# Kernel optimization log

Measured on AMD Instinct MI355X. Metric: run time of the kernel, lower is better.

The kernel has to match this reference:

```python
import jax, jax.numpy as jnp
from jax import lax
import numpy as np

STEPSZ = 0.1
ALPHA = 0.01
BETA = 0.01
FLTRSTD = 2.0
NSTEPS = 20
DMAX = 15.0
EXTGRADFAC = 10.0
CHUNK = 32  # node chunk size for distance-map render


def _gauss_edge_fltr(std):
    # Gaussian-derivative edge filters, one per spatial axis: [2, 1, K, K]
    r = int(np.ceil(3 * std))
    x = np.arange(-r, r + 1, dtype=np.float32)
    g = np.exp(-x ** 2 / (2 * std ** 2)).astype(np.float32)
    g /= g.sum()
    dg = (-x / std ** 2) * g
    f0 = np.outer(dg, g)   # d/d(axis0)
    f1 = np.outer(g, dg)   # d/d(axis1)
    return np.stack([f0, f1])[:, None].astype(np.float32)


def _snake_matrix(n, alpha, beta, stepsz):
    # implicit internal-energy step matrix (I + t*(alpha*D2 + beta*D2@D2))^-1, open chain
    D = 2 * np.eye(n) - np.eye(n, k=1) - np.eye(n, k=-1)
    D[0, 0] = 1.0
    D[-1, -1] = 1.0
    A = alpha * D + beta * (D @ D)
    return np.linalg.inv(np.eye(n) + stepsz * A).astype(np.float32)


def _bilerp(img, pts):
    # img [H,W], pts [N,2] (row, col) -> [N]
    H, W = img.shape
    r = jnp.clip(pts[:, 0], 0.0, H - 1.0)
    c = jnp.clip(pts[:, 1], 0.0, W - 1.0)
    r0 = jnp.floor(r).astype(jnp.int32)
    c0 = jnp.floor(c).astype(jnp.int32)
    r1 = jnp.minimum(r0 + 1, H - 1)
    c1 = jnp.minimum(c0 + 1, W - 1)
    fr = r - r0
    fc = c - c0
    return (img[r0, c0] * (1 - fr) * (1 - fc) + img[r1, c0] * fr * (1 - fc)
            + img[r0, c1] * (1 - fr) * fc + img[r1, c1] * fr * fc)


def setup_inputs() -> dict:
    key = jax.random.key(0)
    k1, k2, k3 = jax.random.split(key, 3)
    B, H, W, N = 8, 512, 512, 256
    pred_dmap = jax.random.normal(k1, (B, 1, H, W), dtype=jnp.float32)
    node_pos = jax.random.uniform(k2, (B, N, 2), dtype=jnp.float32) * jnp.array([H - 1.0, W - 1.0], dtype=jnp.float32)
    widths = jax.random.uniform(k3, (B, N), dtype=jnp.float32) * 3.0 + 1.0
    return {"pred_dmap": pred_dmap, "node_pos": node_pos, "widths": widths}


def reference(pred_dmap, node_pos, widths):
    B, _, H, W = pred_dmap.shape
    N = node_pos.shape[1]

    # gradient image: conv with Gaussian-derivative filters, scaled (cmptGradIm)
    fltr = jnp.asarray(_gauss_edge_fltr(FLTRSTD))
    gimg = lax.conv_general_dilated(
        pred_dmap, fltr, (1, 1), 'SAME',
        dimension_numbers=('NCHW', 'OIHW', 'NCHW')) * EXTGRADFAC  # [B,2,H,W]

    M = jnp.asarray(_snake_matrix(N, ALPHA, BETA, STEPSZ))  # [N,N]

    def force(g, pts):  # g [2,H,W], pts [N,2] -> [N,2]
        return jnp.stack([_bilerp(g[0], pts), _bilerp(g[1], pts)], axis=-1)

    force_b = jax.vmap(force)
    bounds = jnp.array([H - 1.0, W - 1.0], dtype=pred_dmap.dtype)

    def opt_step(pos, _):
        f = force_b(gimg, pos)                                   # [B,N,2]
        pos = jnp.einsum('nm,bmd->bnd', M, pos + STEPSZ * f)
        pos = jnp.clip(pos, 0.0, bounds)
        return pos, None

    pos, _ = lax.scan(opt_step, node_pos, None, length=NSTEPS)

    ys = jnp.arange(H, dtype=pred_dmap.dtype)
    xs = jnp.arange(W, dtype=pred_dmap.dtype)

    def render(p, w):  # p [N,2], w [N] -> [H,W]
        pc = p.reshape(N // CHUNK, CHUNK, 2)
        wc = w.reshape(N // CHUNK, CHUNK)

        def rstep(carry, pw):
            pp, ww = pw  # [C,2], [C]
            d = jnp.sqrt((ys[None, :, None] - pp[:, 0, None, None]) ** 2
                         + (xs[None, None, :] - pp[:, 1, None, None]) ** 2) - ww[:, None, None]
            return jnp.minimum(carry, d.min(0)), None

        dm, _ = lax.scan(rstep, jnp.full((H, W), DMAX, dtype=p.dtype), (pc, wc))
        return jnp.clip(dm, 0.0, DMAX)

    snake_dm = jax.vmap(render)(pos, widths)[:, None]  # [B,1,H,W]
    snake_dm = lax.stop_gradient(snake_dm)             # torch.no_grad in original
    return jnp.mean((pred_dmap - snake_dm) ** 2)
```

## Files before the change

### kernel.cpp

```cpp
#include <hip/hip_runtime.h>
#include <hip/hip_bf16.h>
#include <math.h>

#define HH 512
#define WW 512
#define NB 8
#define NN 256
#define KR 6
#define KS 13

struct MBand { float c[NN][17]; };

constexpr double Dd_c(int i, int j) {
    if (i < 0 || i >= NN || j < 0 || j >= NN) return 0.0;
    if (i == j) return (i == 0 || i == NN - 1) ? 1.0 : 2.0;
    int d = i - j;
    if (d == 1 || d == -1) return -1.0;
    return 0.0;
}

constexpr MBand make_mband() {
    MBand mb{};
    double xb[NN][5] = {};
    for (int n = 0; n < NN; ++n)
        for (int d = 0; d < 5; ++d) {
            int j = n + d - 2;
            double d2 = 0.0;
            for (int k = n - 1; k <= n + 1; ++k) d2 += Dd_c(n, k) * Dd_c(k, j);
            xb[n][d] = 0.1 * (0.01 * Dd_c(n, j) + 0.01 * d2);
        }
    for (int n = 0; n < NN; ++n) {
        double acc[17] = {};
        double cur[17] = {};
        acc[8] = 1.0; cur[8] = 1.0;
        double sign = -1.0;
        for (int k = 1; k <= 4; ++k) {
            double nxt[17] = {};
            int lo = -2 * k, hi = 2 * k;
            for (int tp = lo; tp <= hi; ++tp) {
                int j = n + tp;
                double s = 0.0;
                if (j >= 0 && j < NN) {
                    for (int t = tp - 2; t <= tp + 2; ++t) {
                        if (t < -8 || t > 8) continue;
                        int m = n + t;
                        if (m < 0 || m >= NN) continue;
                        s += cur[8 + t] * xb[m][(tp - t) + 2];
                    }
                }
                nxt[8 + tp] = s;
            }
            for (int q = 0; q < 17; ++q) { cur[q] = nxt[q]; acc[q] += sign * nxt[q]; }
            sign = -sign;
        }
        for (int q = 0; q < 17; ++q) mb.c[n][q] = (float)acc[q];
    }
    return mb;
}

__device__ __constant__ MBand d_mband = make_mband();

union GPix { unsigned u; struct { __hip_bfloat16 x, y; } h; };

__global__ __launch_bounds__(256) void conv_kernel(const float* __restrict__ pred,
                                                   unsigned* __restrict__ gimg,
                                                   float* __restrict__ out) {
    __shared__ float tin[44][44];
    __shared__ float midG[44][32];
    __shared__ float midD[44][32];

    const int b    = blockIdx.x & 7;
    const int tile = blockIdx.x >> 3;
    const int ty0  = (tile >> 4) * 32;
    const int tx0  = (tile & 15) * 32;
    const int t    = threadIdx.x;

    if (blockIdx.x == 0 && t == 0) out[0] = 0.f;

    float g[KS], dg[KS];
    float s = 0.f;
#pragma unroll
    for (int i = 0; i < KS; ++i) {
        float x = (float)(i - KR);
        g[i] = expf(-x * x / 8.f);
        s += g[i];
    }
#pragma unroll
    for (int i = 0; i < KS; ++i) {
        g[i] /= s;
        dg[i] = (-(float)(i - KR) / 4.f) * g[i];
    }

    const float* img = pred + (size_t)b * HH * WW;

    for (int idx = t; idx < 44 * 44; idx += 256) {
        int ly = idx / 44, lx = idx % 44;
        int gy = ty0 + ly - KR, gx = tx0 + lx - KR;
        float v = 0.f;
        if (gy >= 0 && gy < HH && gx >= 0 && gx < WW) v = img[gy * WW + gx];
        tin[ly][lx] = v;
    }
    __syncthreads();

    for (int idx = t; idx < 44 * 32; idx += 256) {
        int ly = idx / 32, ox = idx % 32;
        float aG = 0.f, aD = 0.f;
#pragma unroll
        for (int k = 0; k < KS; ++k) {
            float v = tin[ly][ox + k];
            aG += v * g[k];
            aD += v * dg[k];
        }
        midG[ly][ox] = aG;
        midD[ly][ox] = aD;
    }
    __syncthreads();

    unsigned* outp = gimg + (size_t)b * HH * WW;
    for (int idx = t; idx < 32 * 32; idx += 256) {
        int oy = idx / 32, ox = idx % 32;
        float a0 = 0.f, a1 = 0.f;
#pragma unroll
        for (int k = 0; k < KS; ++k) {
            a0 += midG[oy + k][ox] * dg[k];
            a1 += midD[oy + k][ox] * g[k];
        }
        GPix p;
        p.h.x = __float2bfloat16(10.f * a0);
        p.h.y = __float2bfloat16(10.f * a1);
        outp[(ty0 + oy) * WW + (tx0 + ox)] = p.u;
    }
}

__global__ __launch_bounds__(64, 1) void snake_kernel(const unsigned* __restrict__ gimg,
                                                      const float* __restrict__ node_pos,
                                                      float* __restrict__ pos_out) {
    const int batch = blockIdx.x & 7;
    const int chunk = blockIdx.x >> 3;
    const int l = threadIdx.x;
    const int nidx = chunk * 32 - 8 + l;
    const int cidx = min(max(nidx, 0), NN - 1);

    const unsigned* gp = gimg + (size_t)batch * HH * WW;

    float2 pp = ((const float2*)node_pos)[batch * NN + cidx];
    float p0 = pp.x, p1 = pp.y;

    float mbc[17];
#pragma unroll
    for (int t = 0; t < 17; ++t) mbc[t] = d_mband.c[cidx][t];

    for (int step = 0; step < 20; ++step) {
        float r = fminf(fmaxf(p0, 0.f), (float)(HH - 1));
        float c = fminf(fmaxf(p1, 0.f), (float)(WW - 1));
        float rf = floorf(r), cf = floorf(c);
        int r0 = (int)rf, c0 = (int)cf;
        int r1 = min(r0 + 1, HH - 1), c1 = min(c0 + 1, WW - 1);
        float fr = r - rf, fc = c - cf;
        GPix v00, v01, v10, v11;
        v00.u = gp[r0 * WW + c0];
        v01.u = gp[r0 * WW + c1];
        v10.u = gp[r1 * WW + c0];
        v11.u = gp[r1 * WW + c1];
        float w00 = (1.f - fr) * (1.f - fc), w01 = (1.f - fr) * fc;
        float w10 = fr * (1.f - fc),         w11 = fr * fc;
        float f0 = w00 * __bfloat162float(v00.h.x) + w01 * __bfloat162float(v01.h.x)
                 + w10 * __bfloat162float(v10.h.x) + w11 * __bfloat162float(v11.h.x);
        float f1 = w00 * __bfloat162float(v00.h.y) + w01 * __bfloat162float(v01.h.y)
                 + w10 * __bfloat162float(v10.h.y) + w11 * __bfloat162float(v11.h.y);
        float q0 = p0 + 0.1f * f0;
        float q1 = p1 + 0.1f * f1;

        float a0 = mbc[8] * q0;
        float a1 = mbc[8] * q1;
#pragma unroll
        for (int d = 1; d <= 8; ++d) {
            float u0 = __shfl_up(q0, d),   u1 = __shfl_up(q1, d);
            float w0 = __shfl_down(q0, d), w1 = __shfl_down(q1, d);
            a0 += mbc[8 - d] * u0 + mbc[8 + d] * w0;
            a1 += mbc[8 - d] * u1 + mbc[8 + d] * w1;
        }
        p0 = fminf(fmaxf(a0, 0.f), (float)(HH - 1));
        p1 = fminf(fmaxf(a1, 0.f), (float)(WW - 1));
    }

    if (l >= 8 && l < 40)
        ((float2*)pos_out)[batch * NN + nidx] = make_float2(p0, p1);
}

__global__ __launch_bounds__(256) void render_loss_kernel(const float* __restrict__ pred,
                                                          const float* __restrict__ pos,
                                                          const float* __restrict__ widths,
                                                          float* __restrict__ out) {
    __shared__ float sl0[NN], sl1[NN], slw[NN];
    __shared__ int cnt;
    __shared__ float wred[4];

    const int b    = blockIdx.x & 7;
    const int tile = blockIdx.x >> 3;
    const int ty0  = (tile >> 4) * 32;
    const int tx0  = (tile & 15) * 32;
    const int t    = threadIdx.x;

    if (t == 0) cnt = 0;
    __syncthreads();

    {
        float p0 = pos[(b * NN + t) * 2 + 0];
        float p1 = pos[(b * NN + t) * 2 + 1];
        float w  = widths[b * NN + t];
        float dy = fmaxf(fmaxf((float)ty0 - p0, p0 - (float)(ty0 + 31)), 0.f);
        float dx = fmaxf(fmaxf((float)tx0 - p1, p1 - (float)(tx0 + 31)), 0.f);
        float rr = 15.f + w;
        if (dy * dy + dx * dx <= rr * rr) {
            int i = atomicAdd(&cnt, 1);
            sl0[i] = p0; sl1[i] = p1; slw[i] = w;
        }
    }
    __syncthreads();
    const int c = cnt;

    const int oy = t >> 3;
    const int ox = (t & 7) * 4;
    const float fy = (float)(ty0 + oy);
    const float fx = (float)(tx0 + ox);

    float dm0 = 15.f, dm1 = 15.f, dm2 = 15.f, dm3 = 15.f;
    for (int j = 0; j < c; ++j) {
        float dy  = fy - sl0[j];
        float dy2 = dy * dy;
        float w   = slw[j];
        float dx  = fx - sl1[j];
        dm0 = fminf(dm0, __builtin_amdgcn_sqrtf(dy2 + dx * dx) - w);
        dx += 1.f;
        dm1 = fminf(dm1, __builtin_amdgcn_sqrtf(dy2 + dx * dx) - w);
        dx += 1.f;
        dm2 = fminf(dm2, __builtin_amdgcn_sqrtf(dy2 + dx * dx) - w);
        dx += 1.f;
        dm3 = fminf(dm3, __builtin_amdgcn_sqrtf(dy2 + dx * dx) - w);
    }
    dm0 = fminf(fmaxf(dm0, 0.f), 15.f);
    dm1 = fminf(fmaxf(dm1, 0.f), 15.f);
    dm2 = fminf(fmaxf(dm2, 0.f), 15.f);
    dm3 = fminf(fmaxf(dm3, 0.f), 15.f);

    const float4 pv = *(const float4*)(pred + (size_t)b * HH * WW
                                       + (ty0 + oy) * WW + (tx0 + ox));
    float e0 = pv.x - dm0, e1 = pv.y - dm1, e2 = pv.z - dm2, e3 = pv.w - dm3;
    float acc = (e0 * e0 + e1 * e1 + e2 * e2 + e3 * e3)
              * (1.0f / (float)(NB * HH * WW));

#pragma unroll
    for (int m = 1; m < 64; m <<= 1) acc += __shfl_xor(acc, m);
    if ((t & 63) == 0) wred[t >> 6] = acc;
    __syncthreads();
    if (t == 0) atomicAdd(out, wred[0] + wred[1] + wred[2] + wred[3]);
}

extern "C" void kernel_launch(void* const* d_in, const int* in_sizes, int n_in,
                              void* d_out, int out_size, void* d_ws, size_t ws_size,
                              hipStream_t stream) {
    const float* pred     = (const float*)d_in[0];
    const float* node_pos = (const float*)d_in[1];
    const float* widths   = (const float*)d_in[2];
    float* out = (float*)d_out;

    unsigned* gimg = (unsigned*)d_ws;
    float* pos_out = (float*)d_ws + (size_t)NB * HH * WW;

    conv_kernel<<<NB * 256, 256, 0, stream>>>(pred, gimg, out);

    snake_kernel<<<NB * 8, 64, 0, stream>>>(gimg, node_pos, pos_out);

    render_loss_kernel<<<NB * 256, 256, 0, stream>>>(pred, pos_out, widths, out);
}
```

Baseline: 54.26 us.

## Fuse snake optimization into render kernel with ticket-ordered global-atomic handoff

Merges the snake iteration kernel and the render/loss kernel into one launch. The first 64 blocks, assigned in order through a global ticket counter, run the snake chunks and signal per-batch completion counters. All blocks then spin until their batch's eight chunks are done before rendering. The last block to finish resets the counters. This removes one kernel launch and the gap between launches, and lets render blocks for finished batches start early. In exchange it adds spin-waiting, depends on ticket ordering to avoid deadlock, and keeps global state that persists across calls.

```diff
diff --git a/kernel.cpp b/kernel.cpp
--- a/kernel.cpp
+++ b/kernel.cpp
@@ -8,6 +8,7 @@
 #define NN 256
 #define KR 6
 #define KS 13
+#define NBLK (NB * 256)
 
 struct MBand { float c[NN][17]; };
 
@@ -62,6 +63,10 @@
 
 union GPix { unsigned u; struct { __hip_bfloat16 x, y; } h; };
 
+__device__ unsigned g_ticket = 0;
+__device__ unsigned g_chunk_done[NB] = {};
+__device__ unsigned g_all_done = 0;
+
 __global__ __launch_bounds__(256) void conv_kernel(const float* __restrict__ pred,
                                                    unsigned* __restrict__ gimg,
                                                    float* __restrict__ out) {
@@ -132,129 +137,169 @@
     }
 }
 
-__global__ __launch_bounds__(64, 1) void snake_kernel(const unsigned* __restrict__ gimg,
-                                                      const float* __restrict__ node_pos,
-                                                      float* __restrict__ pos_out) {
-    const int batch = blockIdx.x & 7;
-    const int chunk = blockIdx.x >> 3;
-    const int l = threadIdx.x;
-    const int nidx = chunk * 32 - 8 + l;
-    const int cidx = min(max(nidx, 0), NN - 1);
-
-    const unsigned* gp = gimg + (size_t)batch * HH * WW;
-
-    float2 pp = ((const float2*)node_pos)[batch * NN + cidx];
-    float p0 = pp.x, p1 = pp.y;
-
-    float mbc[17];
-#pragma unroll
-    for (int t = 0; t < 17; ++t) mbc[t] = d_mband.c[cidx][t];
-
-    for (int step = 0; step < 20; ++step) {
-        float r = fminf(fmaxf(p0, 0.f), (float)(HH - 1));
-        float c = fminf(fmaxf(p1, 0.f), (float)(WW - 1));
-        float rf = floorf(r), cf = floorf(c);
-        int r0 = (int)rf, c0 = (int)cf;
-        int r1 = min(r0 + 1, HH - 1), c1 = min(c0 + 1, WW - 1);
-        float fr = r - rf, fc = c - cf;
-        GPix v00, v01, v10, v11;
-        v00.u = gp[r0 * WW + c0];
-        v01.u = gp[r0 * WW + c1];
-        v10.u = gp[r1 * WW + c0];
-        v11.u = gp[r1 * WW + c1];
-        float w00 = (1.f - fr) * (1.f - fc), w01 = (1.f - fr) * fc;
-        float w10 = fr * (1.f - fc),         w11 = fr * fc;
-        float f0 = w00 * __bfloat162float(v00.h.x) + w01 * __bfloat162float(v01.h.x)
-                 + w10 * __bfloat162float(v10.h.x) + w11 * __bfloat162float(v11.h.x);
-        float f1 = w00 * __bfloat162float(v00.h.y) + w01 * __bfloat162float(v01.h.y)
-                 + w10 * __bfloat162float(v10.h.y) + w11 * __bfloat162float(v11.h.y);
-        float q0 = p0 + 0.1f * f0;
-        float q1 = p1 + 0.1f * f1;
-
-        float a0 = mbc[8] * q0;
-        float a1 = mbc[8] * q1;
-#pragma unroll
-        for (int d = 1; d <= 8; ++d) {
-            float u0 = __shfl_up(q0, d),   u1 = __shfl_up(q1, d);
-            float w0 = __shfl_down(q0, d), w1 = __shfl_down(q1, d);
-            a0 += mbc[8 - d] * u0 + mbc[8 + d] * w0;
-            a1 += mbc[8 - d] * u1 + mbc[8 + d] * w1;
-        }
-        p0 = fminf(fmaxf(a0, 0.f), (float)(HH - 1));
-        p1 = fminf(fmaxf(a1, 0.f), (float)(WW - 1));
-    }
-
-    if (l >= 8 && l < 40)
-        ((float2*)pos_out)[batch * NN + nidx] = make_float2(p0, p1);
-}
-
-__global__ __launch_bounds__(256) void render_loss_kernel(const float* __restrict__ pred,
-                                                          const float* __restrict__ pos,
-                                                          const float* __restrict__ widths,
-                                                          float* __restrict__ out) {
+__global__ __launch_bounds__(256) void snake_render_kernel(const float* __restrict__ pred,
+                                                           const unsigned* __restrict__ gimg,
+                                                           const float* __restrict__ node_pos,
+                                                           const float* __restrict__ widths,
+                                                           float* __restrict__ pos_out,
+                                                           float* __restrict__ out) {
     __shared__ float sl0[NN], sl1[NN], slw[NN];
     __shared__ int cnt;
     __shared__ float wred[4];
+    __shared__ unsigned s_ticket;
 
     const int b    = blockIdx.x & 7;
     const int tile = blockIdx.x >> 3;
-    const int ty0  = (tile >> 4) * 32;
-    const int tx0  = (tile & 15) * 32;
     const int t    = threadIdx.x;
 
-    if (t == 0) cnt = 0;
+    if (t == 0)
+        s_ticket = __hip_atomic_fetch_add(&g_ticket, 1u, __ATOMIC_RELAXED,
+                                          __HIP_MEMORY_SCOPE_AGENT);
     __syncthreads();
+    const unsigned tk = s_ticket;
+
+    if (tk < 64u) {
+        const int batch_s = tk & 7;
+        const int chunk   = tk >> 3;
+        if (t < 64) {
+            const int l = t;
+            const int nidx = chunk * 32 - 8 + l;
+            const int cidx = min(max(nidx, 0), NN - 1);
+
+            const unsigned* gp = gimg + (size_t)batch_s * HH * WW;
+
+            float2 pp = ((const float2*)node_pos)[batch_s * NN + cidx];
+            float p0 = pp.x, p1 = pp.y;
+
+            float mbc[17];
+#pragma unroll
+            for (int k = 0; k < 17; ++k) mbc[k] = d_mband.c[cidx][k];
+
+            for (int step = 0; step < 20; ++step) {
+                float r = fminf(fmaxf(p0, 0.f), (float)(HH - 1));
+                float c = fminf(fmaxf(p1, 0.f), (float)(WW - 1));
+                float rf = floorf(r), cf = floorf(c);
+                int r0 = (int)rf, c0 = (int)cf;
+                int r1 = min(r0 + 1, HH - 1), c1 = min(c0 + 1, WW - 1);
+                float fr = r - rf, fc = c - cf;
+                GPix v00, v01, v10, v11;
+                v00.u = gp[r0 * WW + c0];
+                v01.u = gp[r0 * WW + c1];
+                v10.u = gp[r1 * WW + c0];
+                v11.u = gp[r1 * WW + c1];
+                float w00 = (1.f - fr) * (1.f - fc), w01 = (1.f - fr) * fc;
+                float w10 = fr * (1.f - fc),         w11 = fr * fc;
+                float f0 = w00 * __bfloat162float(v00.h.x) + w01 * __bfloat162float(v01.h.x)
+                         + w10 * __bfloat162float(v10.h.x) + w11 * __bfloat162float(v11.h.x);
+                float f1 = w00 * __bfloat162float(v00.h.y) + w01 * __bfloat162float(v01.h.y)
+                         + w10 * __bfloat162float(v10.h.y) + w11 * __bfloat162float(v11.h.y);
+                float q0 = p0 + 0.1f * f0;
+                float q1 = p1 + 0.1f * f1;
+
+                float a0 = mbc[8] * q0;
+                float a1 = mbc[8] * q1;
+#pragma unroll
+                for (int d = 1; d <= 8; ++d) {
+                    float u0 = __shfl_up(q0, d),   u1 = __shfl_up(q1, d);
+                    float w0 = __shfl_down(q0, d), w1 = __shfl_down(q1, d);
+                    a0 += mbc[8 - d] * u0 + mbc[8 + d] * w0;
+                    a1 += mbc[8 - d] * u1 + mbc[8 + d] * w1;
+                }
+                p0 = fminf(fmaxf(a0, 0.f), (float)(HH - 1));
+                p1 = fminf(fmaxf(a1, 0.f), (float)(WW - 1));
+            }
+
+            if (l >= 8 && l < 40)
+                ((float2*)pos_out)[batch_s * NN + nidx] = make_float2(p0, p1);
+        }
+        __syncthreads();
+        if (t == 0)
+            __hip_atomic_fetch_add(&g_chunk_done[batch_s], 1u, __ATOMIC_RELEASE,
+                                   __HIP_MEMORY_SCOPE_AGENT);
+    }
+
+    if (t == 0) {
+        while (__hip_atomic_load(&g_chunk_done[b], __ATOMIC_RELAXED,
+                                 __HIP_MEMORY_SCOPE_AGENT) < 8u)
+            __builtin_amdgcn_s_sleep(16);
+        (void)__hip_atomic_load(&g_chunk_done[b], __ATOMIC_ACQUIRE,
+                                __HIP_MEMORY_SCOPE_AGENT);
+    }
+    __syncthreads();
 
     {
-        float p0 = pos[(b * NN + t) * 2 + 0];
-        float p1 = pos[(b * NN + t) * 2 + 1];
-        float w  = widths[b * NN + t];
-        float dy = fmaxf(fmaxf((float)ty0 - p0, p0 - (float)(ty0 + 31)), 0.f);
-        float dx = fmaxf(fmaxf((float)tx0 - p1, p1 - (float)(tx0 + 31)), 0.f);
-        float rr = 15.f + w;
-        if (dy * dy + dx * dx <= rr * rr) {
-            int i = atomicAdd(&cnt, 1);
-            sl0[i] = p0; sl1[i] = p1; slw[i] = w;
-        }
-    }
-    __syncthreads();
-    const int c = cnt;
-
-    const int oy = t >> 3;
-    const int ox = (t & 7) * 4;
-    const float fy = (float)(ty0 + oy);
-    const float fx = (float)(tx0 + ox);
-
-    float dm0 = 15.f, dm1 = 15.f, dm2 = 15.f, dm3 = 15.f;
-    for (int j = 0; j < c; ++j) {
-        float dy  = fy - sl0[j];
-        float dy2 = dy * dy;
-        float w   = slw[j];
-        float dx  = fx - sl1[j];
-        dm0 = fminf(dm0, __builtin_amdgcn_sqrtf(dy2 + dx * dx) - w);
-        dx += 1.f;
-        dm1 = fminf(dm1, __builtin_amdgcn_sqrtf(dy2 + dx * dx) - w);
-        dx += 1.f;
-        dm2 = fminf(dm2, __builtin_amdgcn_sqrtf(dy2 + dx * dx) - w);
-        dx += 1.f;
-        dm3 = fminf(dm3, __builtin_amdgcn_sqrtf(dy2 + dx * dx) - w);
-    }
-    dm0 = fminf(fmaxf(dm0, 0.f), 15.f);
-    dm1 = fminf(fmaxf(dm1, 0.f), 15.f);
-    dm2 = fminf(fmaxf(dm2, 0.f), 15.f);
-    dm3 = fminf(fmaxf(dm3, 0.f), 15.f);
-
-    const float4 pv = *(const float4*)(pred + (size_t)b * HH * WW
-                                       + (ty0 + oy) * WW + (tx0 + ox));
-    float e0 = pv.x - dm0, e1 = pv.y - dm1, e2 = pv.z - dm2, e3 = pv.w - dm3;
-    float acc = (e0 * e0 + e1 * e1 + e2 * e2 + e3 * e3)
-              * (1.0f / (float)(NB * HH * WW));
-
-#pragma unroll
-    for (int m = 1; m < 64; m <<= 1) acc += __shfl_xor(acc, m);
-    if ((t & 63) == 0) wred[t >> 6] = acc;
-    __syncthreads();
-    if (t == 0) atomicAdd(out, wred[0] + wred[1] + wred[2] + wred[3]);
+        const int ty0 = (tile >> 4) * 32;
+        const int tx0 = (tile & 15) * 32;
+
+        if (t == 0) cnt = 0;
+        __syncthreads();
+
+        {
+            float p0 = pos_out[(b * NN + t) * 2 + 0];
+            float p1 = pos_out[(b * NN + t) * 2 + 1];
+            float w  = widths[b * NN + t];
+            float dy = fmaxf(fmaxf((float)ty0 - p0, p0 - (float)(ty0 + 31)), 0.f);
+            float dx = fmaxf(fmaxf((float)tx0 - p1, p1 - (float)(tx0 + 31)), 0.f);
+            float rr = 15.f + w;
+            if (dy * dy + dx * dx <= rr * rr) {
+                int i = atomicAdd(&cnt, 1);
+                sl0[i] = p0; sl1[i] = p1; slw[i] = w;
+            }
+        }
+        __syncthreads();
+        const int c = cnt;
+
+        const int oy = t >> 3;
+        const int ox = (t & 7) * 4;
+        const float fy = (float)(ty0 + oy);
+        const float fx = (float)(tx0 + ox);
+
+        float dm0 = 15.f, dm1 = 15.f, dm2 = 15.f, dm3 = 15.f;
+        for (int j = 0; j < c; ++j) {
+            float dy  = fy - sl0[j];
+            float dy2 = dy * dy;
+            float w   = slw[j];
+            float dx  = fx - sl1[j];
+            dm0 = fminf(dm0, __builtin_amdgcn_sqrtf(dy2 + dx * dx) - w);
+            dx += 1.f;
+            dm1 = fminf(dm1, __builtin_amdgcn_sqrtf(dy2 + dx * dx) - w);
+            dx += 1.f;
+            dm2 = fminf(dm2, __builtin_amdgcn_sqrtf(dy2 + dx * dx) - w);
+            dx += 1.f;
+            dm3 = fminf(dm3, __builtin_amdgcn_sqrtf(dy2 + dx * dx) - w);
+        }
+        dm0 = fminf(fmaxf(dm0, 0.f), 15.f);
+        dm1 = fminf(fmaxf(dm1, 0.f), 15.f);
+        dm2 = fminf(fmaxf(dm2, 0.f), 15.f);
+        dm3 = fminf(fmaxf(dm3, 0.f), 15.f);
+
+        const float4 pv = *(const float4*)(pred + (size_t)b * HH * WW
+                                           + (ty0 + oy) * WW + (tx0 + ox));
+        float e0 = pv.x - dm0, e1 = pv.y - dm1, e2 = pv.z - dm2, e3 = pv.w - dm3;
+        float acc = (e0 * e0 + e1 * e1 + e2 * e2 + e3 * e3)
+                  * (1.0f / (float)(NB * HH * WW));
+
+#pragma unroll
+        for (int m = 1; m < 64; m <<= 1) acc += __shfl_xor(acc, m);
+        if ((t & 63) == 0) wred[t >> 6] = acc;
+        __syncthreads();
+        if (t == 0) atomicAdd(out, wred[0] + wred[1] + wred[2] + wred[3]);
+    }
+
+    if (t == 0) {
+        unsigned d = __hip_atomic_fetch_add(&g_all_done, 1u, __ATOMIC_ACQ_REL,
+                                            __HIP_MEMORY_SCOPE_AGENT);
+        if (d == NBLK - 1u) {
+            __hip_atomic_store(&g_ticket, 0u, __ATOMIC_RELAXED,
+                               __HIP_MEMORY_SCOPE_AGENT);
+#pragma unroll
+            for (int i = 0; i < NB; ++i)
+                __hip_atomic_store(&g_chunk_done[i], 0u, __ATOMIC_RELAXED,
+                                   __HIP_MEMORY_SCOPE_AGENT);
+            __hip_atomic_store(&g_all_done, 0u, __ATOMIC_RELAXED,
+                               __HIP_MEMORY_SCOPE_AGENT);
+        }
+    }
 }
 
 extern "C" void kernel_launch(void* const* d_in, const int* in_sizes, int n_in,
@@ -270,7 +315,6 @@
 
     conv_kernel<<<NB * 256, 256, 0, stream>>>(pred, gimg, out);
 
-    snake_kernel<<<NB * 8, 64, 0, stream>>>(gimg, node_pos, pos_out);
-
-    render_loss_kernel<<<NB * 256, 256, 0, stream>>>(pred, pos_out, widths, out);
-}
+    snake_render_kernel<<<NBLK, 256, 0, stream>>>(pred, gimg, node_pos, widths,
+                                                  pos_out, out);
+}
```

Measured after the change: 126.3 us. 2.33x slower.
